# Kernel tuning notes

Measured on AMD Instinct MI355X. Metric: run time of the kernel, lower is better.

Reference implementation:

```python
import jax, jax.numpy as jnp
import numpy as np

NUM_CLASSES = 256
WEIGHT = 0.0005
EPS = 1e-12  # torch F.normalize eps


def setup_inputs() -> dict:
    key = jax.random.key(0)
    k1, k2 = jax.random.split(key)
    features = jax.random.normal(k1, (32768, 1024), dtype=jnp.float32)
    labels = jax.random.randint(k2, (32768,), 0, NUM_CLASSES, dtype=jnp.int32)
    return {"features": features, "labels": labels}


def _centroid_loss(features, labels):
    B, D = features.shape
    # row-wise L2 normalize (torch F.normalize: x / max(||x||, eps))
    norms = jnp.linalg.norm(features, axis=1, keepdims=True)
    f = features / jnp.maximum(norms, EPS)

    ones = jnp.ones((B,), f.dtype)
    counts = jax.ops.segment_sum(ones, labels, num_segments=NUM_CLASSES)  # [C]
    sums = jax.ops.segment_sum(f, labels, num_segments=NUM_CLASSES)       # [C, D]

    # rank of each sample within its class (order of first appearance),
    # matching the row order of features[class_mask] in the original loop
    onehot = jax.nn.one_hot(labels, NUM_CLASSES, dtype=jnp.int32)          # [B, C]
    rank = jnp.take_along_axis(jnp.cumsum(onehot, axis=0), labels[:, None].astype(jnp.int32), axis=1)[:, 0] - 1

    # idx_table[c, r] = global index of the r-th member of class c; sentinel B if none
    idx_table = jnp.full((NUM_CLASSES, B), B, dtype=jnp.int32)
    idx_table = idx_table.at[labels, rank].set(jnp.arange(B, dtype=jnp.int32))

    # NOTE: the original code indexes class_features with the GLOBAL index i
    # (arange(n_c) != i), i.e. it excludes the member of the class at position i,
    # and excludes nothing when i >= n_c. We reproduce that exactly.
    arange_b = jnp.arange(B)
    k = idx_table[labels, arange_b]            # class member at in-class position i (global i)
    valid_excl = k < B                          # exclusion only happens when i < class size
    excl_feat = jnp.where(valid_excl[:, None], f[jnp.where(valid_excl, k, 0)], 0.0)

    n_c = counts[labels]                        # class size per sample (float)
    denom = jnp.where(valid_excl, n_c - 1.0, n_c)
    denom = jnp.maximum(denom, 1.0)             # safe for masked-out singleton classes
    centroid = (sums[labels] - excl_feat) / denom[:, None]

    dist = jnp.mean((f - centroid) ** 2, axis=1)  # F.mse_loss(..., reduction='mean')
    contrib = jnp.where(n_c > 1.0, dist, 0.0)     # skip classes with <=1 sample
    return WEIGHT * jnp.sum(contrib) / B


def reference(features, labels):
    return _centroid_loss(features, labels)
```

## Files before the change

kernel.cpp:

```cpp
#include <hip/hip_runtime.h>

#define BN 32768
#define DN 1024
#define CN 256
#define NSLICE 8
#define SROWS (BN / NSLICE)
#define SCAP 56

__device__ __forceinline__ float dot4(float4 a, float4 b) {
    return a.x*b.x + a.y*b.y + a.z*b.z + a.w*b.w;
}

__global__ void __launch_bounds__(256, 8) k_sum(const float4* __restrict__ x4,
                                                const int* __restrict__ labels,
                                                float* __restrict__ sums,
                                                float* __restrict__ rnorm,
                                                int* __restrict__ idx_part,
                                                int* __restrict__ cnt_part) {
    __shared__ unsigned int packed[SROWS / 4];
    __shared__ int lm[SCAP];
    __shared__ int wcnt[4];
    __shared__ float fa[(DN / 4) * 5];

    const int bid = blockIdx.x;
    const int c = bid >> 3;
    const int s = bid & 7;
    const int t = threadIdx.x;
    const int row0 = s * SROWS;

    {
        const int4* l4 = (const int4*)labels + s * (SROWS / 16);
        for (int w = t; w < SROWS / 4; w += 256) {
            const int4 v = ((const int4*)((const int*)labels + row0))[w];
            packed[w] = (unsigned int)(v.x & 255)
                      | ((unsigned int)(v.y & 255) << 8)
                      | ((unsigned int)(v.z & 255) << 16)
                      | ((unsigned int)(v.w & 255) << 24);
        }
        (void)l4;
    }
    for (int i = t; i < (DN / 4) * 5; i += 256) fa[i] = 0.0f;
    __syncthreads();

    const int wave = t >> 6, lane = t & 63;
    const unsigned long long lt = (lane == 0) ? 0ull : (~0ull >> (64 - lane));
    const int ch0 = wave * 16, ch1 = ch0 + 16;

    int cnt = 0;
    for (int ch = ch0; ch < ch1; ++ch) {
        const int gi = ch * 64 + lane;
        const int lab = (packed[gi >> 2] >> ((gi & 3) * 8)) & 255;
        cnt += __popcll(__ballot(lab == c));
    }
    if (lane == 0) wcnt[wave] = cnt;
    __syncthreads();

    int base = 0, ntot = 0;
    for (int w2 = 0; w2 < 4; ++w2) {
        const int v = wcnt[w2];
        if (w2 < wave) base += v;
        ntot += v;
    }

    for (int ch = ch0; ch < ch1; ++ch) {
        const int gi = ch * 64 + lane;
        const int lab = (packed[gi >> 2] >> ((gi & 3) * 8)) & 255;
        const bool pred = (lab == c);
        const unsigned long long mask = __ballot(pred);
        if (pred) {
            const int pos = base + __popcll(mask & lt);
            if (pos < SCAP) {
                const int grow = row0 + gi;
                lm[pos] = grow;
                idx_part[bid * SCAP + pos] = grow;
            }
        }
        base += __popcll(mask);
    }
    if (t == 0) cnt_part[bid] = ntot;
    __syncthreads();

    const int m = min(ntot, SCAP);
    float4 a0 = make_float4(0.f, 0.f, 0.f, 0.f), a1 = a0, a2 = a0, a3 = a0;
    for (int p = wave; p < m; p += 4) {
        const int row = lm[p];
        const float4* b4 = x4 + (size_t)row * 256;
        const float4 v0 = b4[lane];
        const float4 v1 = b4[lane + 64];
        const float4 v2 = b4[lane + 128];
        const float4 v3 = b4[lane + 192];
        float ss = dot4(v0, v0) + dot4(v1, v1) + dot4(v2, v2) + dot4(v3, v3);
#pragma unroll
        for (int off = 32; off; off >>= 1) ss += __shfl_xor(ss, off, 64);
        const float rn = 1.0f / fmaxf(sqrtf(ss), 1e-12f);
        if (lane == 0) rnorm[row] = rn;
        a0.x += v0.x * rn; a0.y += v0.y * rn; a0.z += v0.z * rn; a0.w += v0.w * rn;
        a1.x += v1.x * rn; a1.y += v1.y * rn; a1.z += v1.z * rn; a1.w += v1.w * rn;
        a2.x += v2.x * rn; a2.y += v2.y * rn; a2.z += v2.z * rn; a2.w += v2.w * rn;
        a3.x += v3.x * rn; a3.y += v3.y * rn; a3.z += v3.z * rn; a3.w += v3.w * rn;
    }

    {
        const int q0 = lane, q1 = lane + 64, q2 = lane + 128, q3 = lane + 192;
        atomicAdd(&fa[5 * q0 + 0], a0.x); atomicAdd(&fa[5 * q0 + 1], a0.y);
        atomicAdd(&fa[5 * q0 + 2], a0.z); atomicAdd(&fa[5 * q0 + 3], a0.w);
        atomicAdd(&fa[5 * q1 + 0], a1.x); atomicAdd(&fa[5 * q1 + 1], a1.y);
        atomicAdd(&fa[5 * q1 + 2], a1.z); atomicAdd(&fa[5 * q1 + 3], a1.w);
        atomicAdd(&fa[5 * q2 + 0], a2.x); atomicAdd(&fa[5 * q2 + 1], a2.y);
        atomicAdd(&fa[5 * q2 + 2], a2.z); atomicAdd(&fa[5 * q2 + 3], a2.w);
        atomicAdd(&fa[5 * q3 + 0], a3.x); atomicAdd(&fa[5 * q3 + 1], a3.y);
        atomicAdd(&fa[5 * q3 + 2], a3.z); atomicAdd(&fa[5 * q3 + 3], a3.w);
    }
    __syncthreads();

    {
        float* dst = sums + (size_t)c * DN + 4 * t;
        atomicAdd(dst + 0, fa[5 * t + 0]);
        atomicAdd(dst + 1, fa[5 * t + 1]);
        atomicAdd(dst + 2, fa[5 * t + 2]);
        atomicAdd(dst + 3, fa[5 * t + 3]);
    }
}

__global__ void __launch_bounds__(256) k_finish(const float4* __restrict__ x4,
                                                const float* __restrict__ sums,
                                                const float* __restrict__ rnorm,
                                                const int* __restrict__ idx_part,
                                                const int* __restrict__ cnt_part,
                                                float* __restrict__ out) {
    __shared__ int sic[NSLICE * SCAP];
    __shared__ int scc[NSLICE], spre[NSLICE], sn, snn;
    __shared__ float wred[4];
    __shared__ float4 cred[4];

    const int c = blockIdx.x;
    const int t = threadIdx.x;
    const int wave = t >> 6, lane = t & 63;

    if (t == 0) {
        int n = 0, nn = 0;
        for (int i2 = 0; i2 < NSLICE; ++i2) {
            const int cv = cnt_part[c * NSLICE + i2];
            n += cv;
            const int cc = min(cv, SCAP);
            scc[i2] = cc;
            spre[i2] = nn;
            nn += cc;
        }
        sn = n; snn = nn;
    }
    __syncthreads();
    const int n = sn, nn = snn;
    if (n < 2) return;

    const float4 Sq = ((const float4*)sums)[(size_t)c * 256 + t];

    float d = dot4(Sq, Sq);
#pragma unroll
    for (int off = 32; off; off >>= 1) d += __shfl_xor(d, off, 64);
    if (lane == 0) wred[wave] = d;

    for (int u = t; u < NSLICE * SCAP; u += 256) {
        const int s2i = u / SCAP;
        const int r = u - s2i * SCAP;
        if (r < scc[s2i]) sic[spre[s2i] + r] = idx_part[(c * NSLICE + s2i) * SCAP + r];
    }
    __syncthreads();

    const float s2 = wred[0] + wred[1] + wred[2] + wred[3];
    const int nlim = min(n, nn);

    float dacc = 0.0f;
    for (int p = 0; p < nn; ++p) {
        const int j = sic[p];
        if (j >= nlim) continue;
        const int k = sic[j];
        const float4 xi = x4[(size_t)j * 256 + t];
        const float4 xk = x4[(size_t)k * 256 + t];
        float d0 = dot4(xi, Sq);
        float d1 = dot4(xi, xk);
        float d2 = dot4(xk, Sq);
        float d3 = dot4(xk, xk);
#pragma unroll
        for (int off = 32; off; off >>= 1) {
            d0 += __shfl_xor(d0, off, 64);
            d1 += __shfl_xor(d1, off, 64);
            d2 += __shfl_xor(d2, off, 64);
            d3 += __shfl_xor(d3, off, 64);
        }
        if (lane == 0) cred[wave] = make_float4(d0, d1, d2, d3);
        __syncthreads();
        if (t == 0) {
            const float xiS  = cred[0].x + cred[1].x + cred[2].x + cred[3].x;
            const float xixk = cred[0].y + cred[1].y + cred[2].y + cred[3].y;
            const float xkS  = cred[0].z + cred[1].z + cred[2].z + cred[3].z;
            const float xkxk = cred[0].w + cred[1].w + cred[2].w + cred[3].w;
            const float rni = rnorm[j], rnk = rnorm[k];
            const float fiS  = rni * xiS;
            const float fifk = rni * rnk * xixk;
            const float Sfk  = rnk * xkS;
            const float fk2  = rnk * rnk * xkxk;
            const float nf = (float)n;
            const float dd = nf - 1.0f;
            const float naive = -2.0f * fiS / nf + s2 / (nf * nf);
            const float corr  = -2.0f * (fiS - fifk) / dd + (s2 - 2.0f * Sfk + fk2) / (dd * dd);
            dacc += corr - naive;
        }
        __syncthreads();
    }

    if (t == 0) {
        const float nf = (float)n;
        const float total = (nf - s2 / nf) + dacc;
        atomicAdd(out, total * (1.0f / DN) * (0.0005f / (float)BN));
    }
}

extern "C" void kernel_launch(void* const* d_in, const int* in_sizes, int n_in,
                              void* d_out, int out_size, void* d_ws, size_t ws_size,
                              hipStream_t stream) {
    const float4* x4 = (const float4*)d_in[0];
    const int* labels = (const int*)d_in[1];
    float* out = (float*)d_out;

    char* ws = (char*)d_ws;
    float* sums     = (float*)(ws + 0);
    float* rnorm    = (float*)(ws + 1048576);
    int*   idx_part = (int*)  (ws + 1179648);
    int*   cnt_part = (int*)  (ws + 1638400);

    hipMemsetAsync(sums, 0, (size_t)CN * DN * sizeof(float), stream);
    hipMemsetAsync(out, 0, sizeof(float), stream);
    k_sum<<<CN * NSLICE, 256, 0, stream>>>(x4, labels, sums, rnorm, idx_part, cnt_part);
    k_finish<<<CN, 256, 0, stream>>>(x4, sums, rnorm, idx_part, cnt_part, out);
}
```

Measured before the change: 236.2 us.

## Fuse class-sum and finish kernels into one 1024-thread block per class

Replaces the two-kernel pipeline (256 classes x 8 slices, then a finish kernel) with a single kernel. It launches one 1024-thread block per class, scans all labels in shared memory and keeps member indices and inverse norms in shared memory. This removes the global sums buffer, its memset, the global atomics and the second launch. Each wave also loads two rows per iteration for more memory-level parallelism. The cost is only 256 blocks, with a packed label array of about 32KB per block that may limit occupancy, and the finish loop still runs on 256 of the 1024 threads.

```diff
diff --git a/kernel.cpp b/kernel.cpp
--- a/kernel.cpp
+++ b/kernel.cpp
@@ -3,48 +3,39 @@
 #define BN 32768
 #define DN 1024
 #define CN 256
-#define NSLICE 8
-#define SROWS (BN / NSLICE)
-#define SCAP 56
+#define RCAP 320
 
 __device__ __forceinline__ float dot4(float4 a, float4 b) {
     return a.x*b.x + a.y*b.y + a.z*b.z + a.w*b.w;
 }
 
-__global__ void __launch_bounds__(256, 8) k_sum(const float4* __restrict__ x4,
-                                                const int* __restrict__ labels,
-                                                float* __restrict__ sums,
-                                                float* __restrict__ rnorm,
-                                                int* __restrict__ idx_part,
-                                                int* __restrict__ cnt_part) {
-    __shared__ unsigned int packed[SROWS / 4];
-    __shared__ int lm[SCAP];
-    __shared__ int wcnt[4];
+__global__ void __launch_bounds__(1024) k_all(const float4* __restrict__ x4,
+                                              const int* __restrict__ labels,
+                                              float* __restrict__ out) {
+    __shared__ unsigned int packed[BN / 4];
+    __shared__ int sic[RCAP];
+    __shared__ float rnl[RCAP];
+    __shared__ int wcnt[16];
     __shared__ float fa[(DN / 4) * 5];
+    __shared__ float wred[4];
+    __shared__ float4 cred[4];
 
-    const int bid = blockIdx.x;
-    const int c = bid >> 3;
-    const int s = bid & 7;
+    const int c = blockIdx.x;
     const int t = threadIdx.x;
-    const int row0 = s * SROWS;
 
-    {
-        const int4* l4 = (const int4*)labels + s * (SROWS / 16);
-        for (int w = t; w < SROWS / 4; w += 256) {
-            const int4 v = ((const int4*)((const int*)labels + row0))[w];
-            packed[w] = (unsigned int)(v.x & 255)
-                      | ((unsigned int)(v.y & 255) << 8)
-                      | ((unsigned int)(v.z & 255) << 16)
-                      | ((unsigned int)(v.w & 255) << 24);
-        }
-        (void)l4;
+    for (int w = t; w < BN / 4; w += 1024) {
+        const int4 v = ((const int4*)labels)[w];
+        packed[w] = (unsigned int)(v.x & 255)
+                  | ((unsigned int)(v.y & 255) << 8)
+                  | ((unsigned int)(v.z & 255) << 16)
+                  | ((unsigned int)(v.w & 255) << 24);
     }
-    for (int i = t; i < (DN / 4) * 5; i += 256) fa[i] = 0.0f;
+    for (int i = t; i < (DN / 4) * 5; i += 1024) fa[i] = 0.0f;
     __syncthreads();
 
     const int wave = t >> 6, lane = t & 63;
     const unsigned long long lt = (lane == 0) ? 0ull : (~0ull >> (64 - lane));
-    const int ch0 = wave * 16, ch1 = ch0 + 16;
+    const int ch0 = wave * 32, ch1 = ch0 + 32;
 
     int cnt = 0;
     for (int ch = ch0; ch < ch1; ++ch) {
@@ -56,7 +47,7 @@
     __syncthreads();
 
     int base = 0, ntot = 0;
-    for (int w2 = 0; w2 < 4; ++w2) {
+    for (int w2 = 0; w2 < 16; ++w2) {
         const int v = wcnt[w2];
         if (w2 < wave) base += v;
         ntot += v;
@@ -69,35 +60,50 @@
         const unsigned long long mask = __ballot(pred);
         if (pred) {
             const int pos = base + __popcll(mask & lt);
-            if (pos < SCAP) {
-                const int grow = row0 + gi;
-                lm[pos] = grow;
-                idx_part[bid * SCAP + pos] = grow;
-            }
+            if (pos < RCAP) sic[pos] = gi;
         }
         base += __popcll(mask);
     }
-    if (t == 0) cnt_part[bid] = ntot;
     __syncthreads();
 
-    const int m = min(ntot, SCAP);
+    const int nn = min(ntot, RCAP);
     float4 a0 = make_float4(0.f, 0.f, 0.f, 0.f), a1 = a0, a2 = a0, a3 = a0;
-    for (int p = wave; p < m; p += 4) {
-        const int row = lm[p];
-        const float4* b4 = x4 + (size_t)row * 256;
-        const float4 v0 = b4[lane];
-        const float4 v1 = b4[lane + 64];
-        const float4 v2 = b4[lane + 128];
-        const float4 v3 = b4[lane + 192];
-        float ss = dot4(v0, v0) + dot4(v1, v1) + dot4(v2, v2) + dot4(v3, v3);
+    for (int r = wave; r < nn; r += 32) {
+        const int rowA = sic[r];
+        const bool hasB = (r + 16) < nn;
+        const int rowB = hasB ? sic[r + 16] : rowA;
+        const float4* bA = x4 + (size_t)rowA * 256;
+        const float4* bB = x4 + (size_t)rowB * 256;
+        const float4 uA0 = bA[lane];
+        const float4 uA1 = bA[lane + 64];
+        const float4 uA2 = bA[lane + 128];
+        const float4 uA3 = bA[lane + 192];
+        const float4 uB0 = bB[lane];
+        const float4 uB1 = bB[lane + 64];
+        const float4 uB2 = bB[lane + 128];
+        const float4 uB3 = bB[lane + 192];
+        float sA = dot4(uA0, uA0) + dot4(uA1, uA1) + dot4(uA2, uA2) + dot4(uA3, uA3);
+        float sB = dot4(uB0, uB0) + dot4(uB1, uB1) + dot4(uB2, uB2) + dot4(uB3, uB3);
 #pragma unroll
-        for (int off = 32; off; off >>= 1) ss += __shfl_xor(ss, off, 64);
-        const float rn = 1.0f / fmaxf(sqrtf(ss), 1e-12f);
-        if (lane == 0) rnorm[row] = rn;
-        a0.x += v0.x * rn; a0.y += v0.y * rn; a0.z += v0.z * rn; a0.w += v0.w * rn;
-        a1.x += v1.x * rn; a1.y += v1.y * rn; a1.z += v1.z * rn; a1.w += v1.w * rn;
-        a2.x += v2.x * rn; a2.y += v2.y * rn; a2.z += v2.z * rn; a2.w += v2.w * rn;
-        a3.x += v3.x * rn; a3.y += v3.y * rn; a3.z += v3.z * rn; a3.w += v3.w * rn;
+        for (int off = 32; off; off >>= 1) {
+            sA += __shfl_xor(sA, off, 64);
+            sB += __shfl_xor(sB, off, 64);
+        }
+        const float rnA  = 1.0f / fmaxf(sqrtf(sA), 1e-12f);
+        const float rnBr = 1.0f / fmaxf(sqrtf(sB), 1e-12f);
+        const float rnB  = hasB ? rnBr : 0.0f;
+        if (lane == 0) {
+            rnl[r] = rnA;
+            if (hasB) rnl[r + 16] = rnBr;
+        }
+        a0.x += uA0.x * rnA + uB0.x * rnB; a0.y += uA0.y * rnA + uB0.y * rnB;
+        a0.z += uA0.z * rnA + uB0.z * rnB; a0.w += uA0.w * rnA + uB0.w * rnB;
+        a1.x += uA1.x * rnA + uB1.x * rnB; a1.y += uA1.y * rnA + uB1.y * rnB;
+        a1.z += uA1.z * rnA + uB1.z * rnB; a1.w += uA1.w * rnA + uB1.w * rnB;
+        a2.x += uA2.x * rnA + uB2.x * rnB; a2.y += uA2.y * rnA + uB2.y * rnB;
+        a2.z += uA2.z * rnA + uB2.z * rnB; a2.w += uA2.w * rnA + uB2.w * rnB;
+        a3.x += uA3.x * rnA + uB3.x * rnB; a3.y += uA3.y * rnA + uB3.y * rnB;
+        a3.z += uA3.z * rnA + uB3.z * rnB; a3.w += uA3.w * rnA + uB3.w * rnB;
     }
 
     {
@@ -113,106 +119,70 @@
     }
     __syncthreads();
 
-    {
-        float* dst = sums + (size_t)c * DN + 4 * t;
-        atomicAdd(dst + 0, fa[5 * t + 0]);
-        atomicAdd(dst + 1, fa[5 * t + 1]);
-        atomicAdd(dst + 2, fa[5 * t + 2]);
-        atomicAdd(dst + 3, fa[5 * t + 3]);
+    float4 Sq = make_float4(0.f, 0.f, 0.f, 0.f);
+    float d = 0.0f;
+    if (t < 256) {
+        Sq.x = fa[5 * t + 0]; Sq.y = fa[5 * t + 1];
+        Sq.z = fa[5 * t + 2]; Sq.w = fa[5 * t + 3];
+        d = dot4(Sq, Sq);
     }
-}
-
-__global__ void __launch_bounds__(256) k_finish(const float4* __restrict__ x4,
-                                                const float* __restrict__ sums,
-                                                const float* __restrict__ rnorm,
-                                                const int* __restrict__ idx_part,
-                                                const int* __restrict__ cnt_part,
-                                                float* __restrict__ out) {
-    __shared__ int sic[NSLICE * SCAP];
-    __shared__ int scc[NSLICE], spre[NSLICE], sn, snn;
-    __shared__ float wred[4];
-    __shared__ float4 cred[4];
-
-    const int c = blockIdx.x;
-    const int t = threadIdx.x;
-    const int wave = t >> 6, lane = t & 63;
-
-    if (t == 0) {
-        int n = 0, nn = 0;
-        for (int i2 = 0; i2 < NSLICE; ++i2) {
-            const int cv = cnt_part[c * NSLICE + i2];
-            n += cv;
-            const int cc = min(cv, SCAP);
-            scc[i2] = cc;
-            spre[i2] = nn;
-            nn += cc;
-        }
-        sn = n; snn = nn;
-    }
-    __syncthreads();
-    const int n = sn, nn = snn;
-    if (n < 2) return;
-
-    const float4 Sq = ((const float4*)sums)[(size_t)c * 256 + t];
-
-    float d = dot4(Sq, Sq);
+    if (wave < 4) {
 #pragma unroll
-    for (int off = 32; off; off >>= 1) d += __shfl_xor(d, off, 64);
-    if (lane == 0) wred[wave] = d;
-
-    for (int u = t; u < NSLICE * SCAP; u += 256) {
-        const int s2i = u / SCAP;
-        const int r = u - s2i * SCAP;
-        if (r < scc[s2i]) sic[spre[s2i] + r] = idx_part[(c * NSLICE + s2i) * SCAP + r];
+        for (int off = 32; off; off >>= 1) d += __shfl_xor(d, off, 64);
+        if (lane == 0) wred[wave] = d;
     }
     __syncthreads();
 
-    const float s2 = wred[0] + wred[1] + wred[2] + wred[3];
-    const int nlim = min(n, nn);
-
-    float dacc = 0.0f;
-    for (int p = 0; p < nn; ++p) {
-        const int j = sic[p];
-        if (j >= nlim) continue;
-        const int k = sic[j];
-        const float4 xi = x4[(size_t)j * 256 + t];
-        const float4 xk = x4[(size_t)k * 256 + t];
-        float d0 = dot4(xi, Sq);
-        float d1 = dot4(xi, xk);
-        float d2 = dot4(xk, Sq);
-        float d3 = dot4(xk, xk);
+    const int n = ntot;
+    if (n >= 2) {
+        const float s2 = wred[0] + wred[1] + wred[2] + wred[3];
+        const int nlim = min(n, nn);
+        float dacc = 0.0f;
+        for (int p = 0; p < nn; ++p) {
+            const int j = sic[p];
+            if (j >= nlim) continue;
+            const int k = sic[j];
+            if (t < 256) {
+                const float4 xi = x4[(size_t)j * 256 + t];
+                const float4 xk = x4[(size_t)k * 256 + t];
+                float d0 = dot4(xi, Sq);
+                float d1 = dot4(xi, xk);
+                float d2 = dot4(xk, Sq);
+                float d3 = dot4(xk, xk);
 #pragma unroll
-        for (int off = 32; off; off >>= 1) {
-            d0 += __shfl_xor(d0, off, 64);
-            d1 += __shfl_xor(d1, off, 64);
-            d2 += __shfl_xor(d2, off, 64);
-            d3 += __shfl_xor(d3, off, 64);
+                for (int off = 32; off; off >>= 1) {
+                    d0 += __shfl_xor(d0, off, 64);
+                    d1 += __shfl_xor(d1, off, 64);
+                    d2 += __shfl_xor(d2, off, 64);
+                    d3 += __shfl_xor(d3, off, 64);
+                }
+                if (lane == 0) cred[wave] = make_float4(d0, d1, d2, d3);
+            }
+            __syncthreads();
+            if (t == 0) {
+                const float xiS  = cred[0].x + cred[1].x + cred[2].x + cred[3].x;
+                const float xixk = cred[0].y + cred[1].y + cred[2].y + cred[3].y;
+                const float xkS  = cred[0].z + cred[1].z + cred[2].z + cred[3].z;
+                const float xkxk = cred[0].w + cred[1].w + cred[2].w + cred[3].w;
+                const float rni = rnl[p], rnk = rnl[j];
+                const float fiS  = rni * xiS;
+                const float fifk = rni * rnk * xixk;
+                const float Sfk  = rnk * xkS;
+                const float fk2  = rnk * rnk * xkxk;
+                const float nf = (float)n;
+                const float dd = nf - 1.0f;
+                const float naive = -2.0f * fiS / nf + s2 / (nf * nf);
+                const float corr  = -2.0f * (fiS - fifk) / dd
+                                  + (s2 - 2.0f * Sfk + fk2) / (dd * dd);
+                dacc += corr - naive;
+            }
+            __syncthreads();
         }
-        if (lane == 0) cred[wave] = make_float4(d0, d1, d2, d3);
-        __syncthreads();
         if (t == 0) {
-            const float xiS  = cred[0].x + cred[1].x + cred[2].x + cred[3].x;
-            const float xixk = cred[0].y + cred[1].y + cred[2].y + cred[3].y;
-            const float xkS  = cred[0].z + cred[1].z + cred[2].z + cred[3].z;
-            const float xkxk = cred[0].w + cred[1].w + cred[2].w + cred[3].w;
-            const float rni = rnorm[j], rnk = rnorm[k];
-            const float fiS  = rni * xiS;
-            const float fifk = rni * rnk * xixk;
-            const float Sfk  = rnk * xkS;
-            const float fk2  = rnk * rnk * xkxk;
             const float nf = (float)n;
-            const float dd = nf - 1.0f;
-            const float naive = -2.0f * fiS / nf + s2 / (nf * nf);
-            const float corr  = -2.0f * (fiS - fifk) / dd + (s2 - 2.0f * Sfk + fk2) / (dd * dd);
-            dacc += corr - naive;
+            const float total = (nf - s2 / nf) + dacc;
+            atomicAdd(out, total * (1.0f / DN) * (0.0005f / (float)BN));
         }
-        __syncthreads();
-    }
-
-    if (t == 0) {
-        const float nf = (float)n;
-        const float total = (nf - s2 / nf) + dacc;
-        atomicAdd(out, total * (1.0f / DN) * (0.0005f / (float)BN));
     }
 }
 
@@ -223,14 +193,6 @@
     const int* labels = (const int*)d_in[1];
     float* out = (float*)d_out;
 
-    char* ws = (char*)d_ws;
-    float* sums     = (float*)(ws + 0);
-    float* rnorm    = (float*)(ws + 1048576);
-    int*   idx_part = (int*)  (ws + 1179648);
-    int*   cnt_part = (int*)  (ws + 1638400);
-
-    hipMemsetAsync(sums, 0, (size_t)CN * DN * sizeof(float), stream);
     hipMemsetAsync(out, 0, sizeof(float), stream);
-    k_sum<<<CN * NSLICE, 256, 0, stream>>>(x4, labels, sums, rnorm, idx_part, cnt_part);
-    k_finish<<<CN, 256, 0, stream>>>(x4, sums, rnorm, idx_part, cnt_part, out);
+    k_all<<<CN, 1024, 0, stream>>>(x4, labels, out);
 }
```

Result: faster. 219.6 us (-7.0%).
